# Optimization experiments

Hardware: AMD Instinct MI355X
Metric: run time of the kernel (lower is better)

The kernel has to match this reference:

```python
import jax, jax.numpy as jnp
import numpy as np

B, T, N, F_IN, F_OUT = 8, 64, 256, 128, 64
NEG_INF = -9e15


def setup_inputs() -> dict:
    key = jax.random.key(0)
    k_h, k_w, k_a, k_adj = jax.random.split(key, 4)
    h = jax.random.normal(k_h, (B, T, N, F_IN), dtype=jnp.float32)
    W = jax.random.normal(k_w, (F_IN, F_OUT), dtype=jnp.float32) * (1.414 / np.sqrt(F_IN))
    a = jax.random.normal(k_a, (2 * F_OUT, 1), dtype=jnp.float32) * 0.1
    # binary adjacency with guaranteed self-loops so every softmax row is valid
    adj = (jax.random.uniform(k_adj, (N, N)) > 0.5).astype(jnp.float32)
    adj = jnp.maximum(adj, jnp.eye(N, dtype=jnp.float32))
    return {"h": h, "W": W, "a": a, "adj": adj}


def reference(h, W, a, adj):
    # Wh: [B, T, N, F_OUT]
    Wh = jnp.einsum('btnf,fo->btno', h, W)
    a1 = a[:F_OUT, 0]   # [F_OUT]
    a2 = a[F_OUT:, 0]   # [F_OUT]
    Wh1 = jnp.einsum('btno,o->btn', Wh, a1)  # source scores
    Wh2 = jnp.einsum('btno,o->btn', Wh, a2)  # target scores
    # e: [B, T, N, N] = leakyrelu(Wh1_i + Wh2_j)
    e = jax.nn.leaky_relu(Wh1[..., :, None] + Wh2[..., None, :], negative_slope=0.01)
    attention = jnp.where(adj > 0, e, NEG_INF)
    alpha = jax.nn.softmax(attention, axis=-1)
    # dropout is identity at inference (training=False)
    h_prime = jnp.einsum('btnm,btmo->btno', alpha, Wh)
    return jax.nn.elu(h_prime)  # concat=True path
```

## Files before the change

### kernel.cpp

```cpp
#include <hip/hip_runtime.h>
#include <hip/hip_bf16.h>

#define NN 256
#define FI 128
#define FO 64

typedef short s16x8 __attribute__((ext_vector_type(8)));
typedef float f32x4 __attribute__((ext_vector_type(4)));

__device__ __forceinline__ unsigned f2bf1(float x) {
  union { float f; unsigned u; } v; v.f = x;
  unsigned r = v.u + 0x7FFFu + ((v.u >> 16) & 1u);
  return r >> 16;
}
__device__ __forceinline__ unsigned pack2(float a, float b) {
  return f2bf1(a) | (f2bf1(b) << 16);
}

__global__ __launch_bounds__(256, 4) void gat_k1(
    const float* __restrict__ h, const float* __restrict__ W,
    const float* __restrict__ a,
    unsigned short* __restrict__ whT,
    float* __restrict__ wh1,
    float* __restrict__ wh2)
{
  const int bt   = blockIdx.x >> 2;
  const int tile = blockIdx.x & 3;
  const int tid  = threadIdx.x;
  const int lane = tid & 63;
  const int wv   = tid >> 6;
  const int m    = lane & 15;
  const int q    = lane >> 4;
  const int rw   = tile * 64 + wv * 16;

  __shared__ __align__(16) unsigned short sWT[64 * 136];
  __shared__ __align__(16) float sA[2 * FO];

  const float* __restrict__ hB = h + (size_t)bt * NN * FI;

  float4 x[4][2];
  #pragma unroll
  for (int kt = 0; kt < 4; ++kt) {
    const float* p = hB + (size_t)(rw + m) * FI + kt * 32 + q * 8;
    x[kt][0] = *(const float4*)p;
    x[kt][1] = *(const float4*)(p + 4);
  }

  if (tid < 2 * FO) sA[tid] = a[tid];
  for (int idx = tid; idx < FI * FO; idx += 256) {
    int k = idx >> 6, o = idx & 63;
    sWT[o * 136 + k] = (unsigned short)f2bf1(W[idx]);
  }
  __syncthreads();

  s16x8 af[4];
  #pragma unroll
  for (int kt = 0; kt < 4; ++kt) {
    union { unsigned u[4]; s16x8 v; } pk;
    pk.u[0] = pack2(x[kt][0].x, x[kt][0].y);
    pk.u[1] = pack2(x[kt][0].z, x[kt][0].w);
    pk.u[2] = pack2(x[kt][1].x, x[kt][1].y);
    pk.u[3] = pack2(x[kt][1].z, x[kt][1].w);
    af[kt] = pk.v;
  }

  f32x4 acc[4];
  #pragma unroll
  for (int nt = 0; nt < 4; ++nt) acc[nt] = (f32x4){0.f, 0.f, 0.f, 0.f};
  #pragma unroll
  for (int kt = 0; kt < 4; ++kt) {
    #pragma unroll
    for (int nt = 0; nt < 4; ++nt) {
      s16x8 bf = *(const s16x8*)&sWT[(16 * nt + m) * 136 + kt * 32 + q * 8];
      acc[nt] = __builtin_amdgcn_mfma_f32_16x16x32_bf16(af[kt], bf, acc[nt], 0, 0, 0);
    }
  }

  {
    float p1[4] = {0.f, 0.f, 0.f, 0.f}, p2[4] = {0.f, 0.f, 0.f, 0.f};
    #pragma unroll
    for (int nt = 0; nt < 4; ++nt) {
      float a1v = sA[16 * nt + m];
      float a2v = sA[FO + 16 * nt + m];
      #pragma unroll
      for (int r = 0; r < 4; ++r) {
        p1[r] += acc[nt][r] * a1v;
        p2[r] += acc[nt][r] * a2v;
      }
    }
    #pragma unroll
    for (int off = 1; off < 16; off <<= 1) {
      #pragma unroll
      for (int r = 0; r < 4; ++r) {
        p1[r] += __shfl_xor(p1[r], off);
        p2[r] += __shfl_xor(p2[r], off);
      }
    }
    if (m == 0) {
      float4 v1 = make_float4(p1[0], p1[1], p1[2], p1[3]);
      float4 v2 = make_float4(p2[0], p2[1], p2[2], p2[3]);
      *(float4*)&wh1[bt * NN + rw + 4 * q] = v1;
      *(float4*)&wh2[bt * NN + rw + 4 * q] = v2;
    }
  }

  unsigned short* wB = whT + (size_t)bt * (FO * NN);
  #pragma unroll
  for (int nt = 0; nt < 4; ++nt) {
    int o = 16 * nt + m;
    uint2 wrv;
    wrv.x = pack2(acc[nt][0], acc[nt][1]);
    wrv.y = pack2(acc[nt][2], acc[nt][3]);
    *(uint2*)&wB[o * NN + rw + 4 * q] = wrv;
  }
}

__global__ __launch_bounds__(256, 4) void gat_k2(
    const float* __restrict__ adj,
    const unsigned short* __restrict__ whT,
    const float* __restrict__ wh1, const float* __restrict__ wh2,
    float* __restrict__ out)
{
  const int bt   = blockIdx.x >> 2;
  const int tile = blockIdx.x & 3;
  const int tid  = threadIdx.x;
  const int lane = tid & 63;
  const int wv   = tid >> 6;
  const int m    = lane & 15;
  const int q    = lane >> 4;

  __shared__ __align__(16) unsigned short sWhB[64 * 264];
  __shared__ __align__(16) float sWh2[NN];
  __shared__ __align__(16) float sWh1[64];

  const uint4* src = (const uint4*)(whT + (size_t)bt * (FO * NN));
  uint4 st[8];
  #pragma unroll
  for (int i = 0; i < 8; ++i) st[i] = src[i * 256 + tid];

  sWh2[tid] = wh2[bt * NN + tid];
  if (tid < 64) sWh1[tid] = wh1[bt * NN + tile * 64 + tid];
  __syncthreads();

  const int rw  = tile * 64 + wv * 16;
  const int row = rw + m;
  const float w1 = sWh1[wv * 16 + m];

  s16x8 A[8];
  float sum = 0.f;
  const float* adjr = adj + (size_t)row * NN;
  #pragma unroll
  for (int kt = 0; kt < 8; ++kt) {
    int j0 = kt * 32 + q * 8;
    float4 a0  = *(const float4*)(adjr + j0);
    float4 a1  = *(const float4*)(adjr + j0 + 4);
    float4 w20 = *(const float4*)&sWh2[j0];
    float4 w21 = *(const float4*)&sWh2[j0 + 4];
    float l, p0, p1, p2, p3, p4, p5, p6, p7;
    l = w1 + w20.x; l = fmaxf(l, 0.01f * l); p0 = a0.x > 0.f ? __expf(l) : 0.f;
    l = w1 + w20.y; l = fmaxf(l, 0.01f * l); p1 = a0.y > 0.f ? __expf(l) : 0.f;
    l = w1 + w20.z; l = fmaxf(l, 0.01f * l); p2 = a0.z > 0.f ? __expf(l) : 0.f;
    l = w1 + w20.w; l = fmaxf(l, 0.01f * l); p3 = a0.w > 0.f ? __expf(l) : 0.f;
    l = w1 + w21.x; l = fmaxf(l, 0.01f * l); p4 = a1.x > 0.f ? __expf(l) : 0.f;
    l = w1 + w21.y; l = fmaxf(l, 0.01f * l); p5 = a1.y > 0.f ? __expf(l) : 0.f;
    l = w1 + w21.z; l = fmaxf(l, 0.01f * l); p6 = a1.z > 0.f ? __expf(l) : 0.f;
    l = w1 + w21.w; l = fmaxf(l, 0.01f * l); p7 = a1.w > 0.f ? __expf(l) : 0.f;
    sum += ((p0 + p1) + (p2 + p3)) + ((p4 + p5) + (p6 + p7));
    union { unsigned u[4]; s16x8 v; } pk;
    pk.u[0] = pack2(p0, p1);
    pk.u[1] = pack2(p2, p3);
    pk.u[2] = pack2(p4, p5);
    pk.u[3] = pack2(p6, p7);
    A[kt] = pk.v;
  }
  sum += __shfl_xor(sum, 16);
  sum += __shfl_xor(sum, 32);
  float inv = 1.0f / sum;

  #pragma unroll
  for (int i = 0; i < 8; ++i) {
    int idx = i * 256 + tid;
    int o = idx >> 5, t = idx & 31;
    *(uint4*)&sWhB[o * 264 + t * 8] = st[i];
  }
  __syncthreads();

  f32x4 acc[4];
  #pragma unroll
  for (int nt = 0; nt < 4; ++nt) acc[nt] = (f32x4){0.f, 0.f, 0.f, 0.f};
  #pragma unroll
  for (int kt = 0; kt < 8; ++kt) {
    #pragma unroll
    for (int nt = 0; nt < 4; ++nt) {
      s16x8 bf = *(const s16x8*)&sWhB[(16 * nt + m) * 264 + kt * 32 + q * 8];
      acc[nt] = __builtin_amdgcn_mfma_f32_16x16x32_bf16(A[kt], bf, acc[nt], 0, 0, 0);
    }
  }

  float invr[4];
  #pragma unroll
  for (int r = 0; r < 4; ++r) invr[r] = __shfl(inv, 4 * q + r);
  float* outB = out + (size_t)bt * NN * FO;
  #pragma unroll
  for (int nt = 0; nt < 4; ++nt) {
    int col = 16 * nt + m;
    #pragma unroll
    for (int r = 0; r < 4; ++r) {
      int orow = rw + 4 * q + r;
      float v = acc[nt][r] * invr[r];
      v = v > 0.f ? v : (__expf(v) - 1.f);
      outB[orow * FO + col] = v;
    }
  }
}

extern "C" void kernel_launch(void* const* d_in, const int* in_sizes, int n_in,
                              void* d_out, int out_size, void* d_ws, size_t ws_size,
                              hipStream_t stream) {
  const float* h   = (const float*)d_in[0];
  const float* W   = (const float*)d_in[1];
  const float* a   = (const float*)d_in[2];
  const float* adj = (const float*)d_in[3];
  float* out = (float*)d_out;

  unsigned short* whT = (unsigned short*)d_ws;
  float* wh1 = (float*)((char*)d_ws + (size_t)512 * FO * NN * 2);
  float* wh2 = wh1 + (size_t)512 * NN;

  gat_k1<<<dim3(2048), dim3(256), 0, stream>>>(h, W, a, whT, wh1, wh2);
  gat_k2<<<dim3(2048), dim3(256), 0, stream>>>(adj, whT, wh1, wh2, out);
}
```

Baseline: 153.4 us.

## Bitmask adjacency, async LDS loads, swizzled Wh layout, exp2 softmax, two-subtile K1

Adds a kernel that packs the adjacency into a per-row bitmask, so the attention kernel reads 32 bytes per row instead of 1 KB of floats. K1 now computes two 16-row subtiles per wave over half as many blocks and writes Wh in an XOR-swizzled layout. K2 loads that layout into LDS with global_load_lds directly, removing the register staging and padding. Other changes: exp2 with LOG2E pre-folded into the scores, bitwise masking, truncating bf16 packing, rcp instead of divide, and a reordered block index mapping (bt-major). The extra launch and truncation rounding are the trade-offs.

```diff
diff --git a/kernel.cpp b/kernel.cpp
--- a/kernel.cpp
+++ b/kernel.cpp
@@ -4,6 +4,7 @@
 #define NN 256
 #define FI 128
 #define FO 64
+#define LOG2E 1.4426950408889634f
 
 typedef short s16x8 __attribute__((ext_vector_type(8)));
 typedef float f32x4 __attribute__((ext_vector_type(4)));
@@ -16,43 +17,36 @@
 __device__ __forceinline__ unsigned pack2(float a, float b) {
   return f2bf1(a) | (f2bf1(b) << 16);
 }
-
-__global__ __launch_bounds__(256, 4) void gat_k1(
-    const float* __restrict__ h, const float* __restrict__ W,
-    const float* __restrict__ a,
-    unsigned short* __restrict__ whT,
-    float* __restrict__ wh1,
-    float* __restrict__ wh2)
+__device__ __forceinline__ unsigned pktrunc(float lo, float hi) {
+  union { float f; unsigned u; } a, b; a.f = hi; b.f = lo;
+  return __builtin_amdgcn_perm(a.u, b.u, 0x07060302u);
+}
+__device__ __forceinline__ float fexp2(float x) {
+#if __has_builtin(__builtin_amdgcn_exp2f)
+  return __builtin_amdgcn_exp2f(x);
+#else
+  return exp2f(x);
+#endif
+}
+
+__global__ __launch_bounds__(256) void gat_k0(const float* __restrict__ adj,
+                                              unsigned* __restrict__ msk) {
+  const int row = blockIdx.x;
+  const int wv = threadIdx.x >> 6, lane = threadIdx.x & 63;
+  float v = adj[row * NN + wv * 64 + lane];
+  unsigned long long b = __ballot(v > 0.f);
+  if (lane == 0) {
+    msk[row * 8 + wv * 2]     = (unsigned)b;
+    msk[row * 8 + wv * 2 + 1] = (unsigned)(b >> 32);
+  }
+}
+
+struct K1Out { unsigned short* wB; float* wh1; float* wh2; };
+
+__device__ __forceinline__ void k1_subtile(
+    const float4 (&x)[4][2], int rw, int m, int q,
+    const unsigned short* sWT, const float* sA, int bt, K1Out o_)
 {
-  const int bt   = blockIdx.x >> 2;
-  const int tile = blockIdx.x & 3;
-  const int tid  = threadIdx.x;
-  const int lane = tid & 63;
-  const int wv   = tid >> 6;
-  const int m    = lane & 15;
-  const int q    = lane >> 4;
-  const int rw   = tile * 64 + wv * 16;
-
-  __shared__ __align__(16) unsigned short sWT[64 * 136];
-  __shared__ __align__(16) float sA[2 * FO];
-
-  const float* __restrict__ hB = h + (size_t)bt * NN * FI;
-
-  float4 x[4][2];
-  #pragma unroll
-  for (int kt = 0; kt < 4; ++kt) {
-    const float* p = hB + (size_t)(rw + m) * FI + kt * 32 + q * 8;
-    x[kt][0] = *(const float4*)p;
-    x[kt][1] = *(const float4*)(p + 4);
-  }
-
-  if (tid < 2 * FO) sA[tid] = a[tid];
-  for (int idx = tid; idx < FI * FO; idx += 256) {
-    int k = idx >> 6, o = idx & 63;
-    sWT[o * 136 + k] = (unsigned short)f2bf1(W[idx]);
-  }
-  __syncthreads();
-
   s16x8 af[4];
   #pragma unroll
   for (int kt = 0; kt < 4; ++kt) {
@@ -63,126 +57,169 @@
     pk.u[3] = pack2(x[kt][1].z, x[kt][1].w);
     af[kt] = pk.v;
   }
-
   f32x4 acc[4];
   #pragma unroll
   for (int nt = 0; nt < 4; ++nt) acc[nt] = (f32x4){0.f, 0.f, 0.f, 0.f};
   #pragma unroll
-  for (int kt = 0; kt < 4; ++kt) {
+  for (int kt = 0; kt < 4; ++kt)
     #pragma unroll
     for (int nt = 0; nt < 4; ++nt) {
       s16x8 bf = *(const s16x8*)&sWT[(16 * nt + m) * 136 + kt * 32 + q * 8];
       acc[nt] = __builtin_amdgcn_mfma_f32_16x16x32_bf16(af[kt], bf, acc[nt], 0, 0, 0);
     }
-  }
 
   {
-    float p1[4] = {0.f, 0.f, 0.f, 0.f}, p2[4] = {0.f, 0.f, 0.f, 0.f};
+    float p1[4] = {0.f,0.f,0.f,0.f}, p2[4] = {0.f,0.f,0.f,0.f};
     #pragma unroll
     for (int nt = 0; nt < 4; ++nt) {
       float a1v = sA[16 * nt + m];
       float a2v = sA[FO + 16 * nt + m];
       #pragma unroll
-      for (int r = 0; r < 4; ++r) {
-        p1[r] += acc[nt][r] * a1v;
-        p2[r] += acc[nt][r] * a2v;
-      }
-    }
-    #pragma unroll
-    for (int off = 1; off < 16; off <<= 1) {
+      for (int r = 0; r < 4; ++r) { p1[r] += acc[nt][r] * a1v; p2[r] += acc[nt][r] * a2v; }
+    }
+    #pragma unroll
+    for (int off = 1; off < 16; off <<= 1)
       #pragma unroll
       for (int r = 0; r < 4; ++r) {
         p1[r] += __shfl_xor(p1[r], off);
         p2[r] += __shfl_xor(p2[r], off);
       }
-    }
     if (m == 0) {
-      float4 v1 = make_float4(p1[0], p1[1], p1[2], p1[3]);
-      float4 v2 = make_float4(p2[0], p2[1], p2[2], p2[3]);
-      *(float4*)&wh1[bt * NN + rw + 4 * q] = v1;
-      *(float4*)&wh2[bt * NN + rw + 4 * q] = v2;
-    }
-  }
-
-  unsigned short* wB = whT + (size_t)bt * (FO * NN);
-  #pragma unroll
-  for (int nt = 0; nt < 4; ++nt) {
-    int o = 16 * nt + m;
-    uint2 wrv;
-    wrv.x = pack2(acc[nt][0], acc[nt][1]);
-    wrv.y = pack2(acc[nt][2], acc[nt][3]);
-    *(uint2*)&wB[o * NN + rw + 4 * q] = wrv;
-  }
-}
-
-__global__ __launch_bounds__(256, 4) void gat_k2(
-    const float* __restrict__ adj,
-    const unsigned short* __restrict__ whT,
-    const float* __restrict__ wh1, const float* __restrict__ wh2,
-    float* __restrict__ out)
+      *(float4*)&o_.wh1[bt * NN + rw + 4 * q] =
+          make_float4(p1[0]*LOG2E, p1[1]*LOG2E, p1[2]*LOG2E, p1[3]*LOG2E);
+      *(float4*)&o_.wh2[bt * NN + rw + 4 * q] =
+          make_float4(p2[0]*LOG2E, p2[1]*LOG2E, p2[2]*LOG2E, p2[3]*LOG2E);
+    }
+  }
+  {
+    int t  = (rw >> 3) + (q >> 1);
+    int eo = (q & 1) * 4;
+    #pragma unroll
+    for (int nt = 0; nt < 4; ++nt) {
+      int o = 16 * nt + m;
+      int c = t ^ (o & 7);
+      uint2 wrv;
+      wrv.x = pack2(acc[nt][0], acc[nt][1]);
+      wrv.y = pack2(acc[nt][2], acc[nt][3]);
+      *(uint2*)&o_.wB[o * NN + c * 8 + eo] = wrv;
+    }
+  }
+}
+
+__global__ __launch_bounds__(256, 4) void gat_k1(
+    const float* __restrict__ h, const float* __restrict__ W,
+    const float* __restrict__ a,
+    unsigned short* __restrict__ whT, float* __restrict__ wh1,
+    float* __restrict__ wh2)
 {
-  const int bt   = blockIdx.x >> 2;
-  const int tile = blockIdx.x & 3;
+  const int bt   = blockIdx.x & 511;
+  const int tile = blockIdx.x >> 9;
   const int tid  = threadIdx.x;
   const int lane = tid & 63;
   const int wv   = tid >> 6;
   const int m    = lane & 15;
   const int q    = lane >> 4;
-
-  __shared__ __align__(16) unsigned short sWhB[64 * 264];
-  __shared__ __align__(16) float sWh2[NN];
-  __shared__ __align__(16) float sWh1[64];
-
-  const uint4* src = (const uint4*)(whT + (size_t)bt * (FO * NN));
-  uint4 st[8];
-  #pragma unroll
-  for (int i = 0; i < 8; ++i) st[i] = src[i * 256 + tid];
-
-  sWh2[tid] = wh2[bt * NN + tid];
-  if (tid < 64) sWh1[tid] = wh1[bt * NN + tile * 64 + tid];
+  const int rw0  = tile * 128 + wv * 32;
+
+  __shared__ __align__(16) unsigned short sWT[64 * 136];
+  __shared__ __align__(16) float sA[2 * FO];
+
+  const float* __restrict__ hB = h + (size_t)bt * NN * FI;
+
+  float4 x0[4][2], x1[4][2];
+  #pragma unroll
+  for (int kt = 0; kt < 4; ++kt) {
+    const float* p = hB + (size_t)(rw0 + m) * FI + kt * 32 + q * 8;
+    x0[kt][0] = *(const float4*)p; x0[kt][1] = *(const float4*)(p + 4);
+  }
+  #pragma unroll
+  for (int kt = 0; kt < 4; ++kt) {
+    const float* p = hB + (size_t)(rw0 + 16 + m) * FI + kt * 32 + q * 8;
+    x1[kt][0] = *(const float4*)p; x1[kt][1] = *(const float4*)(p + 4);
+  }
+
+  if (tid < 2 * FO) sA[tid] = a[tid];
+  for (int idx = tid; idx < FI * FO; idx += 256) {
+    int k = idx >> 6, o = idx & 63;
+    sWT[o * 136 + k] = (unsigned short)f2bf1(W[idx]);
+  }
   __syncthreads();
+
+  K1Out o_{ whT + (size_t)bt * (FO * NN), wh1, wh2 };
+  k1_subtile(x0, rw0,      m, q, sWT, sA, bt, o_);
+  k1_subtile(x1, rw0 + 16, m, q, sWT, sA, bt, o_);
+}
+
+__global__ __launch_bounds__(256, 4) void gat_k2(
+    const unsigned* __restrict__ msk,
+    const unsigned short* __restrict__ whT,
+    const float* __restrict__ wh1, const float* __restrict__ wh2,
+    float* __restrict__ out)
+{
+  const int bt   = blockIdx.x & 511;
+  const int tile = blockIdx.x >> 9;
+  const int tid  = threadIdx.x;
+  const int lane = tid & 63;
+  const int wv   = tid >> 6;
+  const int m    = lane & 15;
+  const int q    = lane >> 4;
+
+  __shared__ __align__(16) unsigned short sWhB[64 * 256];
+  __shared__ __align__(16) float sW2[4][256];
+
+  const unsigned short* wg = whT + (size_t)bt * (FO * NN);
+  #pragma unroll
+  for (int i = 0; i < 8; ++i) {
+    const unsigned short* gp = wg + (size_t)(i * 256 + tid) * 8;
+    unsigned short* lp = &sWhB[(i * 256 + wv * 64) * 8];
+    __builtin_amdgcn_global_load_lds(
+        (const __attribute__((address_space(1))) unsigned int*)gp,
+        (__attribute__((address_space(3))) unsigned int*)lp, 16, 0, 0);
+  }
+
+  {
+    float4 w2 = *(const float4*)&wh2[bt * NN + 4 * lane];
+    *(float4*)&sW2[wv][4 * lane] = w2;
+  }
 
   const int rw  = tile * 64 + wv * 16;
   const int row = rw + m;
-  const float w1 = sWh1[wv * 16 + m];
+  const float w1 = wh1[bt * NN + row];
+
+  const uint4 mka = *(const uint4*)&msk[row * 8];
+  const uint4 mkb = *(const uint4*)&msk[row * 8 + 4];
+  const unsigned mkw[8] = {mka.x, mka.y, mka.z, mka.w, mkb.x, mkb.y, mkb.z, mkb.w};
 
   s16x8 A[8];
   float sum = 0.f;
-  const float* adjr = adj + (size_t)row * NN;
   #pragma unroll
   for (int kt = 0; kt < 8; ++kt) {
     int j0 = kt * 32 + q * 8;
-    float4 a0  = *(const float4*)(adjr + j0);
-    float4 a1  = *(const float4*)(adjr + j0 + 4);
-    float4 w20 = *(const float4*)&sWh2[j0];
-    float4 w21 = *(const float4*)&sWh2[j0 + 4];
-    float l, p0, p1, p2, p3, p4, p5, p6, p7;
-    l = w1 + w20.x; l = fmaxf(l, 0.01f * l); p0 = a0.x > 0.f ? __expf(l) : 0.f;
-    l = w1 + w20.y; l = fmaxf(l, 0.01f * l); p1 = a0.y > 0.f ? __expf(l) : 0.f;
-    l = w1 + w20.z; l = fmaxf(l, 0.01f * l); p2 = a0.z > 0.f ? __expf(l) : 0.f;
-    l = w1 + w20.w; l = fmaxf(l, 0.01f * l); p3 = a0.w > 0.f ? __expf(l) : 0.f;
-    l = w1 + w21.x; l = fmaxf(l, 0.01f * l); p4 = a1.x > 0.f ? __expf(l) : 0.f;
-    l = w1 + w21.y; l = fmaxf(l, 0.01f * l); p5 = a1.y > 0.f ? __expf(l) : 0.f;
-    l = w1 + w21.z; l = fmaxf(l, 0.01f * l); p6 = a1.z > 0.f ? __expf(l) : 0.f;
-    l = w1 + w21.w; l = fmaxf(l, 0.01f * l); p7 = a1.w > 0.f ? __expf(l) : 0.f;
-    sum += ((p0 + p1) + (p2 + p3)) + ((p4 + p5) + (p6 + p7));
+    float4 w20 = *(const float4*)&sW2[wv][j0];
+    float4 w21 = *(const float4*)&sW2[wv][j0 + 4];
+    unsigned wq = mkw[kt] >> (q * 8);
+    float p[8];
+    const float w2e[8] = {w20.x, w20.y, w20.z, w20.w, w21.x, w21.y, w21.z, w21.w};
+    #pragma unroll
+    for (int e = 0; e < 8; ++e) {
+      float l = w1 + w2e[e];
+      l = fmaxf(l, 0.01f * l);
+      union { float f; int i; } u_; u_.f = fexp2(l);
+      u_.i &= ((int)(wq << (31 - e))) >> 31;
+      p[e] = u_.f;
+      sum += u_.f;
+    }
     union { unsigned u[4]; s16x8 v; } pk;
-    pk.u[0] = pack2(p0, p1);
-    pk.u[1] = pack2(p2, p3);
-    pk.u[2] = pack2(p4, p5);
-    pk.u[3] = pack2(p6, p7);
+    pk.u[0] = pktrunc(p[0], p[1]);
+    pk.u[1] = pktrunc(p[2], p[3]);
+    pk.u[2] = pktrunc(p[4], p[5]);
+    pk.u[3] = pktrunc(p[6], p[7]);
     A[kt] = pk.v;
   }
   sum += __shfl_xor(sum, 16);
   sum += __shfl_xor(sum, 32);
-  float inv = 1.0f / sum;
-
-  #pragma unroll
-  for (int i = 0; i < 8; ++i) {
-    int idx = i * 256 + tid;
-    int o = idx >> 5, t = idx & 31;
-    *(uint4*)&sWhB[o * 264 + t * 8] = st[i];
-  }
+  const float inv = __builtin_amdgcn_rcpf(sum);
+
   __syncthreads();
 
   f32x4 acc[4];
@@ -190,9 +227,11 @@
   for (int nt = 0; nt < 4; ++nt) acc[nt] = (f32x4){0.f, 0.f, 0.f, 0.f};
   #pragma unroll
   for (int kt = 0; kt < 8; ++kt) {
-    #pragma unroll
-    for (int nt = 0; nt < 4; ++nt) {
-      s16x8 bf = *(const s16x8*)&sWhB[(16 * nt + m) * 264 + kt * 32 + q * 8];
+    int t = kt * 4 + q;
+    #pragma unroll
+    for (int nt = 0; nt < 4; ++nt) {
+      int o = 16 * nt + m;
+      s16x8 bf = *(const s16x8*)&sWhB[o * NN + ((t ^ (o & 7)) * 8)];
       acc[nt] = __builtin_amdgcn_mfma_f32_16x16x32_bf16(A[kt], bf, acc[nt], 0, 0, 0);
     }
   }
@@ -208,7 +247,8 @@
     for (int r = 0; r < 4; ++r) {
       int orow = rw + 4 * q + r;
       float v = acc[nt][r] * invr[r];
-      v = v > 0.f ? v : (__expf(v) - 1.f);
+      float ev = fexp2(v * LOG2E) - 1.f;
+      v = v > 0.f ? v : ev;
       outB[orow * FO + col] = v;
     }
   }
@@ -226,7 +266,9 @@
   unsigned short* whT = (unsigned short*)d_ws;
   float* wh1 = (float*)((char*)d_ws + (size_t)512 * FO * NN * 2);
   float* wh2 = wh1 + (size_t)512 * NN;
-
-  gat_k1<<<dim3(2048), dim3(256), 0, stream>>>(h, W, a, whT, wh1, wh2);
-  gat_k2<<<dim3(2048), dim3(256), 0, stream>>>(adj, whT, wh1, wh2, out);
-}
+  unsigned* msk = (unsigned*)(wh2 + (size_t)512 * NN);
+
+  gat_k0<<<dim3(256),  dim3(256), 0, stream>>>(adj, msk);
+  gat_k1<<<dim3(1024), dim3(256), 0, stream>>>(h, W, a, whT, wh1, wh2);
+  gat_k2<<<dim3(2048), dim3(256), 0, stream>>>(msk, whT, wh1, wh2, out);
+}
```

New measurement: 141.4 us. 7.8% less time.
